# Performance work log

Hardware: AMD Instinct MI355X
Metric: run time of the kernel (lower is better)

Reference implementation:

```python
import jax, jax.numpy as jnp
import numpy as np

N, S, I, F, M = 1024, 8, 128, 1024, 512


def setup_inputs() -> dict:
    key = jax.random.key(0)
    ks = jax.random.split(key, 16)
    sc_x = 0.02  # weight init scale (gain details don't change the op structure)
    d = {
        "modulation": jax.random.normal(ks[0], (N, S * I), dtype=jnp.float32),
        # per-gate grouped weights: input-proj [S, F, I], hidden-proj [S, F, F], bias [S, F]
        "Wxi": jax.random.normal(ks[1], (S, F, I), dtype=jnp.float32) * sc_x,
        "Whi": jax.random.normal(ks[2], (S, F, F), dtype=jnp.float32) * sc_x,
        "bi": jnp.full((S, F), -1.0, dtype=jnp.float32),  # init_input
        "Wxf": jax.random.normal(ks[3], (S, F, I), dtype=jnp.float32) * sc_x,
        "Whf": jax.random.normal(ks[4], (S, F, F), dtype=jnp.float32) * sc_x,
        "bf": jnp.full((S, F), 1.0, dtype=jnp.float32),  # init_forget
        "Wxg": jax.random.normal(ks[5], (S, F, I), dtype=jnp.float32) * sc_x,
        "Whg": jax.random.normal(ks[6], (S, F, F), dtype=jnp.float32) * sc_x,
        "bg": jnp.zeros((S, F), dtype=jnp.float32),
        "Wxo": jax.random.normal(ks[7], (S, F, I), dtype=jnp.float32) * sc_x,
        "Who": jax.random.normal(ks[8], (S, F, F), dtype=jnp.float32) * sc_x,
        "bo": jnp.zeros((S, F), dtype=jnp.float32),
        # out projection [S, M, F] + bias
        "Wout": jax.random.normal(ks[9], (S, M, F), dtype=jnp.float32) * sc_x,
        "bout": jnp.zeros((S, M), dtype=jnp.float32),
    }
    return d


def reference(modulation, Wxi, Whi, bi, Wxf, Whf, bf, Wxg, Whg, bg, Wxo, Who, bo, Wout, bout):
    x = modulation.reshape(N, S, I)  # grouped per-stream input
    # first call: no past state -> h = c = zeros([1, S*F]) (broadcasts over N)
    h0 = jnp.zeros((1, S, F), dtype=modulation.dtype)
    c0 = jnp.zeros((1, S, F), dtype=modulation.dtype)

    def gate(Wx, Wh, b):
        # Accumulate([Linear(x), Linear(h)]): block-diagonal (grouped) matmuls
        return (jnp.einsum('nsi,sfi->nsf', x, Wx)
                + jnp.einsum('msf,sgf->msg', h0, Wh)
                + b)

    i = jax.nn.sigmoid(gate(Wxi, Whi, bi))
    f = jax.nn.sigmoid(gate(Wxf, Whf, bf))
    g = jnp.tanh(gate(Wxg, Whg, bg))
    o = jax.nn.sigmoid(gate(Wxo, Who, bo))
    c = f * c0 + i * g            # [N, S, F]
    h = o * jnp.tanh(c)           # [N, S, F]  (dropout p=0 -> identity)
    out = jnp.einsum('nsf,smf->nsm', h, Wout) + bout  # [N, S, M]
    return out.reshape(N, S * M)
```

## Files before the change

kernel.cpp:

```cpp
#include <hip/hip_runtime.h>

#define N_ 1024
#define S_ 8
#define I_ 128
#define F_ 1024
#define M_ 512

typedef unsigned short ushort_t;
typedef __attribute__((ext_vector_type(8))) short bf16x8;
typedef __attribute__((ext_vector_type(4))) float f32x4;

__device__ __forceinline__ unsigned short f2bf(float x) {
    unsigned int u = __float_as_uint(x);
    u += 0x7fffu + ((u >> 16) & 1u);
    return (unsigned short)(u >> 16);
}

__device__ __forceinline__ float sigmoidf_(float x) {
    return 1.f / (1.f + __expf(-x));
}
__device__ __forceinline__ float tanhf_(float x) {
    float xc = fminf(fmaxf(x, -15.f), 15.f);
    float e = __expf(2.f * xc);
    return (e - 1.f) / (e + 1.f);
}

__device__ __forceinline__ void gload_lds16(const ushort_t* g, ushort_t* l) {
    __builtin_amdgcn_global_load_lds((const __attribute__((address_space(1))) void*)g,
                                     (__attribute__((address_space(3))) void*)l, 16, 0, 0);
}

__global__ __launch_bounds__(256) void k_convert(
    const float* __restrict__ mod, const float* __restrict__ wxi,
    const float* __restrict__ wxg, const float* __restrict__ wxo,
    const float* __restrict__ wout, ushort_t* __restrict__ ws) {
    unsigned v = blockIdx.x * 256u + threadIdx.x;
    const float4* src; unsigned idx; ushort_t* dst;
    if (v < 262144u)       { src = (const float4*)mod;  idx = v;            dst = ws; }
    else if (v < 524288u)  { src = (const float4*)wxi;  idx = v - 262144u;  dst = ws + 1048576; }
    else if (v < 786432u)  { src = (const float4*)wxg;  idx = v - 524288u;  dst = ws + 2097152; }
    else if (v < 1048576u) { src = (const float4*)wxo;  idx = v - 786432u;  dst = ws + 3145728; }
    else                   { src = (const float4*)wout; idx = v - 1048576u; dst = ws + 4194304; }
    float4 f = src[idx];
    ushort4 o;
    o.x = f2bf(f.x); o.y = f2bf(f.y); o.z = f2bf(f.z); o.w = f2bf(f.w);
    ((ushort4*)dst)[idx] = o;
}

__global__ __launch_bounds__(256, 2) void k_gates(
    const ushort_t* __restrict__ xb, const ushort_t* __restrict__ wib,
    const ushort_t* __restrict__ wgb, const ushort_t* __restrict__ wob,
    const float* __restrict__ bi, const float* __restrict__ bg,
    const float* __restrict__ bo, ushort_t* __restrict__ hb) {
    const int s  = blockIdx.z;
    const int n0 = blockIdx.y * 128;
    const int f0 = blockIdx.x * 64;
    __shared__ ushort_t sA[128 * 64];
    __shared__ ushort_t sB[3][64 * 64];
    const int tid  = threadIdx.x;
    const int lane = tid & 63;
    const int w    = tid >> 6;
    const int wm   = (w >> 1) * 64;
    const int wn   = (w & 1) * 32;

    f32x4 acc[3][4][2];
    #pragma unroll
    for (int g = 0; g < 3; ++g)
        #pragma unroll
        for (int mt = 0; mt < 4; ++mt)
            #pragma unroll
            for (int nt = 0; nt < 2; ++nt)
                acc[g][mt][nt] = (f32x4){0.f, 0.f, 0.f, 0.f};

    const ushort_t* wb0 = wib + (size_t)s * (F_ * I_);
    const ushort_t* wb1 = wgb + (size_t)s * (F_ * I_);
    const ushort_t* wb2 = wob + (size_t)s * (F_ * I_);

    for (int k0 = 0; k0 < 128; k0 += 64) {
        #pragma unroll
        for (int i = 0; i < 4; ++i) {
            int c = tid + i * 256;
            int row = c >> 3, kc = c & 7;
            gload_lds16(xb + (size_t)(n0 + row) * (S_ * I_) + s * I_ + k0 + kc * 8, sA + c * 8);
        }
        #pragma unroll
        for (int i = 0; i < 2; ++i) {
            int c = tid + i * 256;
            int row = c >> 3, kc = c & 7;
            size_t goff = (size_t)(f0 + row) * I_ + k0 + kc * 8;
            gload_lds16(wb0 + goff, &sB[0][c * 8]);
            gload_lds16(wb1 + goff, &sB[1][c * 8]);
            gload_lds16(wb2 + goff, &sB[2][c * 8]);
        }
        __syncthreads();
        #pragma unroll
        for (int kk = 0; kk < 2; ++kk) {
            const int kb = kk * 32 + (lane >> 4) * 8;
            bf16x8 a[4];
            #pragma unroll
            for (int mt = 0; mt < 4; ++mt)
                a[mt] = *(const bf16x8*)(sA + (wm + mt * 16 + (lane & 15)) * 64 + kb);
            #pragma unroll
            for (int g = 0; g < 3; ++g) {
                #pragma unroll
                for (int nt = 0; nt < 2; ++nt) {
                    bf16x8 b = *(const bf16x8*)(&sB[g][(wn + nt * 16 + (lane & 15)) * 64 + kb]);
                    #pragma unroll
                    for (int mt = 0; mt < 4; ++mt)
                        acc[g][mt][nt] = __builtin_amdgcn_mfma_f32_16x16x32_bf16(
                            a[mt], b, acc[g][mt][nt], 0, 0, 0);
                }
            }
        }
        __syncthreads();
    }

    const int q = lane >> 4, cl = lane & 15;
    #pragma unroll
    for (int nt = 0; nt < 2; ++nt) {
        int fc = f0 + wn + nt * 16 + cl;
        float bii = bi[s * F_ + fc], bgg = bg[s * F_ + fc], boo = bo[s * F_ + fc];
        #pragma unroll
        for (int mt = 0; mt < 4; ++mt) {
            #pragma unroll
            for (int r = 0; r < 4; ++r) {
                int nr = n0 + wm + mt * 16 + q * 4 + r;
                float pi = acc[0][mt][nt][r] + bii;
                float pg = acc[1][mt][nt][r] + bgg;
                float po = acc[2][mt][nt][r] + boo;
                float hv = sigmoidf_(po) * tanhf_(sigmoidf_(pi) * tanhf_(pg));
                hb[(size_t)s * (N_ * F_) + (size_t)nr * F_ + fc] = f2bf(hv);
            }
        }
    }
}

__global__ __launch_bounds__(256, 2) void k_out(
    const ushort_t* __restrict__ hb, const ushort_t* __restrict__ woutb,
    const float* __restrict__ bout, float* __restrict__ out) {
    const int s  = blockIdx.z;
    const int n0 = blockIdx.y * 128;
    const int m0 = blockIdx.x * 128;
    __shared__ ushort_t sA[128 * 64];
    __shared__ ushort_t sB[128 * 64];
    const int tid = threadIdx.x, lane = tid & 63, w = tid >> 6;
    const int wm = (w >> 1) * 64, wn = (w & 1) * 64;

    f32x4 acc[4][4];
    #pragma unroll
    for (int mt = 0; mt < 4; ++mt)
        #pragma unroll
        for (int nt = 0; nt < 4; ++nt)
            acc[mt][nt] = (f32x4){0.f, 0.f, 0.f, 0.f};

    const ushort_t* ha = hb + (size_t)s * (N_ * F_);
    const ushort_t* wa = woutb + (size_t)s * (M_ * F_);

    for (int k0 = 0; k0 < 1024; k0 += 64) {
        #pragma unroll
        for (int i = 0; i < 4; ++i) {
            int c = tid + i * 256;
            int row = c >> 3, kc = c & 7;
            gload_lds16(ha + (size_t)(n0 + row) * F_ + k0 + kc * 8, sA + c * 8);
            gload_lds16(wa + (size_t)(m0 + row) * F_ + k0 + kc * 8, sB + c * 8);
        }
        __syncthreads();
        #pragma unroll
        for (int kk = 0; kk < 2; ++kk) {
            const int kb = kk * 32 + (lane >> 4) * 8;
            bf16x8 a[4], b[4];
            #pragma unroll
            for (int mt = 0; mt < 4; ++mt)
                a[mt] = *(const bf16x8*)(sA + (wm + mt * 16 + (lane & 15)) * 64 + kb);
            #pragma unroll
            for (int nt = 0; nt < 4; ++nt)
                b[nt] = *(const bf16x8*)(sB + (wn + nt * 16 + (lane & 15)) * 64 + kb);
            #pragma unroll
            for (int nt = 0; nt < 4; ++nt)
                #pragma unroll
                for (int mt = 0; mt < 4; ++mt)
                    acc[mt][nt] = __builtin_amdgcn_mfma_f32_16x16x32_bf16(
                        a[mt], b[nt], acc[mt][nt], 0, 0, 0);
        }
        __syncthreads();
    }

    const int q = lane >> 4, cl = lane & 15;
    #pragma unroll
    for (int nt = 0; nt < 4; ++nt) {
        int mc = m0 + wn + nt * 16 + cl;
        float bb = bout[s * M_ + mc];
        #pragma unroll
        for (int mt = 0; mt < 4; ++mt) {
            #pragma unroll
            for (int r = 0; r < 4; ++r) {
                int nr = n0 + wm + mt * 16 + q * 4 + r;
                out[(size_t)nr * (S_ * M_) + s * M_ + mc] = acc[mt][nt][r] + bb;
            }
        }
    }
}

extern "C" void kernel_launch(void* const* d_in, const int* in_sizes, int n_in,
                              void* d_out, int out_size, void* d_ws, size_t ws_size,
                              hipStream_t stream) {
    const float* mod  = (const float*)d_in[0];
    const float* Wxi  = (const float*)d_in[1];
    const float* bi   = (const float*)d_in[3];
    const float* Wxg  = (const float*)d_in[7];
    const float* bg   = (const float*)d_in[9];
    const float* Wxo  = (const float*)d_in[10];
    const float* bo   = (const float*)d_in[12];
    const float* Wout = (const float*)d_in[13];
    const float* bout = (const float*)d_in[14];

    ushort_t* ws  = (ushort_t*)d_ws;
    ushort_t* xb  = ws;
    ushort_t* wib = ws + 1048576;
    ushort_t* wgb = ws + 2097152;
    ushort_t* wob = ws + 3145728;
    ushort_t* wtb = ws + 4194304;
    ushort_t* hb  = ws + 8388608;

    k_convert<<<8192, 256, 0, stream>>>(mod, Wxi, Wxg, Wxo, Wout, ws);
    k_gates<<<dim3(16, 8, 8), 256, 0, stream>>>(xb, wib, wgb, wob, bi, bg, bo, hb);
    k_out<<<dim3(4, 8, 8), 256, 0, stream>>>(hb, wtb, bout, (float*)d_out);
}
```

Measured before the change: 220.0 us.

## Pad LDS rows to avoid bank conflicts and retile k_out to 128x64 with K=128

Both GEMM kernels now pad their shared-memory rows (64->72 and 128->136 bf16). The padding is filled by issuing extra direct-to-LDS loads of a duplicated chunk, which keeps the row layout compatible with global_load_lds. This is meant to remove bank conflicts on the bf16x8 fragment reads. k_out also switches from 128x128 tiles with K step 64 to 128x64 tiles with K step 128, doubling the grid to 512 blocks for better CU occupancy. In exchange, the A tile is reloaded by twice as many blocks, and the index math now uses divisions by 9 and 17.

Result: no change. 221.3 us (+0.6%).

```diff
diff --git a/kernel.cpp b/kernel.cpp
--- a/kernel.cpp
+++ b/kernel.cpp
@@ -55,10 +55,12 @@
     const int s  = blockIdx.z;
     const int n0 = blockIdx.y * 128;
     const int f0 = blockIdx.x * 64;
-    __shared__ ushort_t sA[128 * 64];
-    __shared__ ushort_t sB[3][64 * 64];
+    __shared__ ushort_t sA[128 * 72];
+    __shared__ ushort_t sB[3][64 * 72];
     const int tid  = threadIdx.x;
     const int lane = tid & 63;
+    const int cl   = lane & 15;
+    const int quad = lane >> 4;
     const int w    = tid >> 6;
     const int wm   = (w >> 1) * 64;
     const int wn   = (w & 1) * 32;
@@ -78,33 +80,40 @@
 
     for (int k0 = 0; k0 < 128; k0 += 64) {
         #pragma unroll
-        for (int i = 0; i < 4; ++i) {
-            int c = tid + i * 256;
-            int row = c >> 3, kc = c & 7;
-            gload_lds16(xb + (size_t)(n0 + row) * (S_ * I_) + s * I_ + k0 + kc * 8, sA + c * 8);
-        }
-        #pragma unroll
-        for (int i = 0; i < 2; ++i) {
-            int c = tid + i * 256;
-            int row = c >> 3, kc = c & 7;
-            size_t goff = (size_t)(f0 + row) * I_ + k0 + kc * 8;
-            gload_lds16(wb0 + goff, &sB[0][c * 8]);
-            gload_lds16(wb1 + goff, &sB[1][c * 8]);
-            gload_lds16(wb2 + goff, &sB[2][c * 8]);
+        for (int i = 0; i < 5; ++i) {
+            unsigned c = (unsigned)tid + i * 256u;
+            if (c < 1152u) {
+                unsigned row = c / 9u, kc = c % 9u;
+                unsigned kce = kc < 8u ? kc : 7u;
+                gload_lds16(xb + (size_t)(n0 + row) * (S_ * I_) + s * I_ + k0 + kce * 8,
+                            sA + c * 8);
+            }
+        }
+        #pragma unroll
+        for (int i = 0; i < 3; ++i) {
+            unsigned c = (unsigned)tid + i * 256u;
+            if (c < 576u) {
+                unsigned row = c / 9u, kc = c % 9u;
+                unsigned kce = kc < 8u ? kc : 7u;
+                size_t goff = (size_t)(f0 + row) * I_ + k0 + kce * 8;
+                gload_lds16(wb0 + goff, &sB[0][c * 8]);
+                gload_lds16(wb1 + goff, &sB[1][c * 8]);
+                gload_lds16(wb2 + goff, &sB[2][c * 8]);
+            }
         }
         __syncthreads();
         #pragma unroll
         for (int kk = 0; kk < 2; ++kk) {
-            const int kb = kk * 32 + (lane >> 4) * 8;
+            const int kb = kk * 32 + quad * 8;
             bf16x8 a[4];
             #pragma unroll
             for (int mt = 0; mt < 4; ++mt)
-                a[mt] = *(const bf16x8*)(sA + (wm + mt * 16 + (lane & 15)) * 64 + kb);
+                a[mt] = *(const bf16x8*)(sA + (wm + mt * 16 + cl) * 72 + kb);
             #pragma unroll
             for (int g = 0; g < 3; ++g) {
                 #pragma unroll
                 for (int nt = 0; nt < 2; ++nt) {
-                    bf16x8 b = *(const bf16x8*)(&sB[g][(wn + nt * 16 + (lane & 15)) * 64 + kb]);
+                    bf16x8 b = *(const bf16x8*)(&sB[g][(wn + nt * 16 + cl) * 72 + kb]);
                     #pragma unroll
                     for (int mt = 0; mt < 4; ++mt)
                         acc[g][mt][nt] = __builtin_amdgcn_mfma_f32_16x16x32_bf16(
@@ -115,7 +124,6 @@
         __syncthreads();
     }
 
-    const int q = lane >> 4, cl = lane & 15;
     #pragma unroll
     for (int nt = 0; nt < 2; ++nt) {
         int fc = f0 + wn + nt * 16 + cl;
@@ -124,7 +132,7 @@
         for (int mt = 0; mt < 4; ++mt) {
             #pragma unroll
             for (int r = 0; r < 4; ++r) {
-                int nr = n0 + wm + mt * 16 + q * 4 + r;
+                int nr = n0 + wm + mt * 16 + quad * 4 + r;
                 float pi = acc[0][mt][nt][r] + bii;
                 float pg = acc[1][mt][nt][r] + bgg;
                 float po = acc[2][mt][nt][r] + boo;
@@ -140,43 +148,59 @@
     const float* __restrict__ bout, float* __restrict__ out) {
     const int s  = blockIdx.z;
     const int n0 = blockIdx.y * 128;
-    const int m0 = blockIdx.x * 128;
-    __shared__ ushort_t sA[128 * 64];
-    __shared__ ushort_t sB[128 * 64];
-    const int tid = threadIdx.x, lane = tid & 63, w = tid >> 6;
-    const int wm = (w >> 1) * 64, wn = (w & 1) * 64;
-
-    f32x4 acc[4][4];
+    const int m0 = blockIdx.x * 64;
+    __shared__ ushort_t sA[128 * 136];
+    __shared__ ushort_t sB[64 * 136];
+    const int tid  = threadIdx.x;
+    const int lane = tid & 63;
+    const int cl   = lane & 15;
+    const int quad = lane >> 4;
+    const int w    = tid >> 6;
+    const int wm   = (w >> 1) * 64;
+    const int wn   = (w & 1) * 32;
+
+    f32x4 acc[4][2];
     #pragma unroll
     for (int mt = 0; mt < 4; ++mt)
         #pragma unroll
-        for (int nt = 0; nt < 4; ++nt)
+        for (int nt = 0; nt < 2; ++nt)
             acc[mt][nt] = (f32x4){0.f, 0.f, 0.f, 0.f};
 
     const ushort_t* ha = hb + (size_t)s * (N_ * F_);
     const ushort_t* wa = woutb + (size_t)s * (M_ * F_);
 
-    for (int k0 = 0; k0 < 1024; k0 += 64) {
-        #pragma unroll
-        for (int i = 0; i < 4; ++i) {
-            int c = tid + i * 256;
-            int row = c >> 3, kc = c & 7;
-            gload_lds16(ha + (size_t)(n0 + row) * F_ + k0 + kc * 8, sA + c * 8);
-            gload_lds16(wa + (size_t)(m0 + row) * F_ + k0 + kc * 8, sB + c * 8);
-        }
-        __syncthreads();
-        #pragma unroll
-        for (int kk = 0; kk < 2; ++kk) {
-            const int kb = kk * 32 + (lane >> 4) * 8;
-            bf16x8 a[4], b[4];
+    for (int k0 = 0; k0 < 1024; k0 += 128) {
+        #pragma unroll
+        for (int i = 0; i < 9; ++i) {
+            unsigned c = (unsigned)tid + i * 256u;
+            if (c < 2176u) {
+                unsigned row = c / 17u, kc = c % 17u;
+                unsigned kce = kc < 16u ? kc : 15u;
+                gload_lds16(ha + (size_t)(n0 + row) * F_ + k0 + kce * 8, sA + c * 8);
+            }
+        }
+        #pragma unroll
+        for (int i = 0; i < 5; ++i) {
+            unsigned c = (unsigned)tid + i * 256u;
+            if (c < 1088u) {
+                unsigned row = c / 17u, kc = c % 17u;
+                unsigned kce = kc < 16u ? kc : 15u;
+                gload_lds16(wa + (size_t)(m0 + row) * F_ + k0 + kce * 8, sB + c * 8);
+            }
+        }
+        __syncthreads();
+        #pragma unroll
+        for (int kk = 0; kk < 4; ++kk) {
+            const int kb = kk * 32 + quad * 8;
+            bf16x8 a[4], b[2];
             #pragma unroll
             for (int mt = 0; mt < 4; ++mt)
-                a[mt] = *(const bf16x8*)(sA + (wm + mt * 16 + (lane & 15)) * 64 + kb);
-            #pragma unroll
-            for (int nt = 0; nt < 4; ++nt)
-                b[nt] = *(const bf16x8*)(sB + (wn + nt * 16 + (lane & 15)) * 64 + kb);
-            #pragma unroll
-            for (int nt = 0; nt < 4; ++nt)
+                a[mt] = *(const bf16x8*)(sA + (wm + mt * 16 + cl) * 136 + kb);
+            #pragma unroll
+            for (int nt = 0; nt < 2; ++nt)
+                b[nt] = *(const bf16x8*)(sB + (wn + nt * 16 + cl) * 136 + kb);
+            #pragma unroll
+            for (int nt = 0; nt < 2; ++nt)
                 #pragma unroll
                 for (int mt = 0; mt < 4; ++mt)
                     acc[mt][nt] = __builtin_amdgcn_mfma_f32_16x16x32_bf16(
@@ -185,16 +209,15 @@
         __syncthreads();
     }
 
-    const int q = lane >> 4, cl = lane & 15;
-    #pragma unroll
-    for (int nt = 0; nt < 4; ++nt) {
+    #pragma unroll
+    for (int nt = 0; nt < 2; ++nt) {
         int mc = m0 + wn + nt * 16 + cl;
         float bb = bout[s * M_ + mc];
         #pragma unroll
         for (int mt = 0; mt < 4; ++mt) {
             #pragma unroll
             for (int r = 0; r < 4; ++r) {
-                int nr = n0 + wm + mt * 16 + q * 4 + r;
+                int nr = n0 + wm + mt * 16 + quad * 4 + r;
                 out[(size_t)nr * (S_ * M_) + s * M_ + mc] = acc[mt][nt][r] + bb;
             }
         }
@@ -224,5 +247,5 @@
 
     k_convert<<<8192, 256, 0, stream>>>(mod, Wxi, Wxg, Wxo, Wout, ws);
     k_gates<<<dim3(16, 8, 8), 256, 0, stream>>>(xb, wib, wgb, wob, bi, bg, bo, hb);
-    k_out<<<dim3(4, 8, 8), 256, 0, stream>>>(hb, wtb, bout, (float*)d_out);
-}
+    k_out<<<dim3(8, 8, 8), 256, 0, stream>>>(hb, wtb, bout, (float*)d_out);
+}
```
